# Kernel tuning notes

Measured on AMD Instinct MI355X. Metric: run time of the kernel, lower is better.

The kernel has to match this reference:

```python
import jax, jax.numpy as jnp
import numpy as np

B, S, H, I, E, K = 4, 2048, 1024, 4096, 8, 2


def setup_inputs() -> dict:
    key = jax.random.key(0)
    ks = jax.random.split(key, 5)
    scale = 1.0 / np.sqrt(H)
    return {
        "hidden_states": jax.random.normal(ks[0], (B, S, H), dtype=jnp.float32),
        "router_w": jax.random.normal(ks[1], (E, H), dtype=jnp.float32) * scale,
        "gate_w": jax.random.normal(ks[2], (E, I, H), dtype=jnp.float32) * scale,
        "up_w": jax.random.normal(ks[3], (E, I, H), dtype=jnp.float32) * scale,
        "down_w": jax.random.normal(ks[4], (E, H, I), dtype=jnp.float32) * (1.0 / np.sqrt(I)),
        "top_k": K,
    }


def reference(hidden_states, router_w, gate_w, up_w, down_w, top_k):
    # Router: logits -> softmax -> top-k -> renormalized weights (eval mode, no jitter)
    logits = jnp.einsum("bsh,eh->bse", hidden_states, router_w)
    probs = jax.nn.softmax(logits, axis=-1)
    expert_weights, expert_indices = jax.lax.top_k(probs, top_k)  # [B,S,K]
    expert_weights = expert_weights / expert_weights.sum(axis=-1, keepdims=True)

    n_experts = router_w.shape[0]
    # Per-token combine weight for each expert: [B,S,E]
    combine = (jax.nn.one_hot(expert_indices, n_experts, dtype=expert_weights.dtype)
               * expert_weights[..., None]).sum(axis=-2)

    out = jnp.zeros_like(hidden_states)
    for e in range(n_experts):  # fixed small expert count
        g = jax.nn.silu(hidden_states @ gate_w[e].T)  # [B,S,I]
        u = hidden_states @ up_w[e].T                 # [B,S,I]
        y = (g * u) @ down_w[e].T                     # [B,S,H]
        out = out + combine[..., e:e + 1] * y
    return out
```

## Files before the change

kernel.cpp:

```cpp
#include <hip/hip_runtime.h>
#include <hip/hip_bf16.h>
#include <math.h>
#include <stdint.h>

#define TOKENS 8192
#define HD 1024
#define ID 4096
#define NE 8
#define RMAX 18432
#define MAXT 72

typedef __attribute__((ext_vector_type(8))) short short8v;
typedef __attribute__((ext_vector_type(4))) float f32x4;

typedef const __attribute__((address_space(1))) unsigned int* gas_u32p;
typedef __attribute__((address_space(3))) unsigned int* las_u32p;

__device__ __forceinline__ void stage16(const void* g, void* l) {
  __builtin_amdgcn_global_load_lds((gas_u32p)g, (las_u32p)l, 16, 0, 0);
}

#define BARRIER asm volatile("s_barrier" ::: "memory")
#define WAITLGKM asm volatile("s_waitcnt lgkmcnt(0)" ::: "memory")
#define VMC0 asm volatile("s_waitcnt vmcnt(0)" ::: "memory")
#define VMC3 asm volatile("s_waitcnt vmcnt(3)" ::: "memory")
#define VMC6 asm volatile("s_waitcnt vmcnt(6)" ::: "memory")

__global__ __launch_bounds__(256) void convert_kernel(const float* __restrict__ src,
                                                      __hip_bfloat16* __restrict__ dst) {
  size_t i = ((size_t)blockIdx.x * 256 + threadIdx.x) * 8;
  float4 a = ((const float4*)(src + i))[0];
  float4 b = ((const float4*)(src + i))[1];
  union { __hip_bfloat16 h[8]; int4 v; } u;
  u.h[0] = __float2bfloat16(a.x); u.h[1] = __float2bfloat16(a.y);
  u.h[2] = __float2bfloat16(a.z); u.h[3] = __float2bfloat16(a.w);
  u.h[4] = __float2bfloat16(b.x); u.h[5] = __float2bfloat16(b.y);
  u.h[6] = __float2bfloat16(b.z); u.h[7] = __float2bfloat16(b.w);
  *(int4*)(dst + i) = u.v;
}

__global__ __launch_bounds__(256) void router_kernel(
    const float* __restrict__ h, const float* __restrict__ rw,
    __hip_bfloat16* __restrict__ hx, int* __restrict__ tidx,
    float* __restrict__ tw, int* __restrict__ cnt) {
  int wid = threadIdx.x >> 6, lane = threadIdx.x & 63;
  int t = blockIdx.x * 4 + wid;
  const float4* h4 = (const float4*)(h + (size_t)t * HD);
  float x[16];
  {
    float4 xa = h4[lane * 4 + 0], xb = h4[lane * 4 + 1], xc = h4[lane * 4 + 2], xd = h4[lane * 4 + 3];
    x[0] = xa.x; x[1] = xa.y; x[2] = xa.z; x[3] = xa.w;
    x[4] = xb.x; x[5] = xb.y; x[6] = xb.z; x[7] = xb.w;
    x[8] = xc.x; x[9] = xc.y; x[10] = xc.z; x[11] = xc.w;
    x[12] = xd.x; x[13] = xd.y; x[14] = xd.z; x[15] = xd.w;
  }
  union { __hip_bfloat16 hb[16]; int4 v[2]; } u;
#pragma unroll
  for (int j = 0; j < 16; j++) u.hb[j] = __float2bfloat16(x[j]);
  {
    int4* hxp = (int4*)(hx + (size_t)t * HD + lane * 16);
    hxp[0] = u.v[0]; hxp[1] = u.v[1];
  }
  double acc[NE];
#pragma unroll
  for (int e = 0; e < NE; e++) {
    const float4* w4 = (const float4*)(rw + e * HD);
    float4 wa = w4[lane * 4 + 0], wb = w4[lane * 4 + 1], wc = w4[lane * 4 + 2], wd = w4[lane * 4 + 3];
    double s = 0.0;
    s += (double)x[0] * wa.x + (double)x[1] * wa.y + (double)x[2] * wa.z + (double)x[3] * wa.w;
    s += (double)x[4] * wb.x + (double)x[5] * wb.y + (double)x[6] * wb.z + (double)x[7] * wb.w;
    s += (double)x[8] * wc.x + (double)x[9] * wc.y + (double)x[10] * wc.z + (double)x[11] * wc.w;
    s += (double)x[12] * wd.x + (double)x[13] * wd.y + (double)x[14] * wd.z + (double)x[15] * wd.w;
    acc[e] = s;
  }
#pragma unroll
  for (int off = 32; off >= 1; off >>= 1)
#pragma unroll
    for (int e = 0; e < NE; e++) acc[e] += __shfl_xor(acc[e], off, 64);
  if (lane == 0) {
    int i0 = 0; double l0 = acc[0];
#pragma unroll
    for (int e = 1; e < NE; e++) if (acc[e] > l0) { l0 = acc[e]; i0 = e; }
    int i1 = -1; double l1 = -1.0e300;
#pragma unroll
    for (int e = 0; e < NE; e++) if (e != i0 && acc[e] > l1) { l1 = acc[e]; i1 = e; }
    double r = exp(l1 - l0);
    float w0 = (float)(1.0 / (1.0 + r));
    float w1 = (float)(r / (1.0 + r));
    tidx[t * 2 + 0] = i0; tidx[t * 2 + 1] = i1;
    tw[t * 2 + 0] = w0;  tw[t * 2 + 1] = w1;
    atomicAdd(&cnt[i0], 1); atomicAdd(&cnt[i1], 1);
  }
}

__global__ void scan_kernel(const int* __restrict__ cnt, int* __restrict__ ofs, int* __restrict__ cnt2) {
  if (threadIdx.x == 0) {
    int a = 0;
    for (int e = 0; e < NE; e++) { ofs[e] = a; a += (cnt[e] + 255) & ~255; }
    ofs[NE] = a;
  }
  if (threadIdx.x < NE) cnt2[threadIdx.x] = 0;
}

__global__ __launch_bounds__(256) void scatter_kernel(
    const int* __restrict__ tidx, const float* __restrict__ tw,
    const int* __restrict__ ofs, int* __restrict__ cnt2,
    int* __restrict__ rowmap, int* __restrict__ slots) {
  int t = blockIdx.x * 256 + threadIdx.x;
#pragma unroll
  for (int k = 0; k < 2; k++) {
    int e = tidx[t * 2 + k];
    int pos = atomicAdd(&cnt2[e], 1);
    int row = ofs[e] + pos;
    rowmap[row] = t;
    slots[t * 2 + k] = row;
  }
}

#define MFMAQ(ACC, MO, NO, AF, BF)                                                         \
  { _Pragma("unroll") for (int m_ = 0; m_ < 4; m_++)                                       \
    _Pragma("unroll") for (int n_ = 0; n_ < 2; n_++)                                       \
    _Pragma("unroll") for (int k_ = 0; k_ < 2; k_++)                                       \
      ACC[(MO) + m_][(NO) + n_] = __builtin_amdgcn_mfma_f32_16x16x32_bf16(                 \
          AF[m_][k_], BF[n_][k_], ACC[(MO) + m_][(NO) + n_], 0, 0, 0); }

__global__ __launch_bounds__(512, 2) void gemm1_kernel(
    const __hip_bfloat16* __restrict__ hx, const __hip_bfloat16* __restrict__ Wg,
    const __hip_bfloat16* __restrict__ Wu, const int* __restrict__ rowmap,
    const int* __restrict__ ofs, const __hip_bfloat16* __restrict__ zrow,
    __hip_bfloat16* __restrict__ act) {
  __shared__ __align__(128) char lds[131072];
  const int nwg = gridDim.x;
  int wg0 = blockIdx.x;
  int wg = (wg0 & 7) * (nwg >> 3) + (wg0 >> 3);
  const int tm = wg >> 5, tn = wg & 31;
  const int Rtot = ofs[NE];
  const int row0 = tm * 256;
  if (row0 >= Rtot) return;
  int e = 0;
#pragma unroll
  for (int i = 1; i < NE; i++) e += (row0 >= ofs[i]);
  const int tid = threadIdx.x, wid = tid >> 6, lane = tid & 63;
  const int wm = wid >> 1, wn = wid & 1;
  const int fr = lane & 15, fkE = (lane >> 4) << 3;
  const int wmB = wm * 64, wnB = wn * 64;

  const char* srcA[4]; const char* srcG[2]; const char* srcU[2];
  int ldA[4], ldG[2], ldU[2];
#pragma unroll
  for (int j = 0; j < 4; j++) {
    int d = j * 8192 + tid * 16;
    int row = d >> 7;
    int kb = (d ^ (((d >> 7) & 7) << 4)) & 127;
    int tok = rowmap[row0 + row];
    const __hip_bfloat16* base = (tok >= 0) ? (hx + (size_t)tok * HD) : zrow;
    srcA[j] = (const char*)base + kb;
    ldA[j] = j * 8192 + wid * 1024;
  }
#pragma unroll
  for (int j = 0; j < 2; j++) {
    int d = j * 8192 + tid * 16;
    int row = d >> 7;
    int kb = (d ^ (((d >> 7) & 7) << 4)) & 127;
    srcG[j] = (const char*)(Wg + ((size_t)e * ID + tn * 128 + row) * HD) + kb;
    srcU[j] = (const char*)(Wu + ((size_t)e * ID + tn * 128 + row) * HD) + kb;
    ldG[j] = 32768 + j * 8192 + wid * 1024;
    ldU[j] = 49152 + j * 8192 + wid * 1024;
  }
#define STG_A(j, t, bf) stage16(srcA[j] + (size_t)(t) * 128, (char*)lds + (bf) * 65536 + ldA[j])
#define STG_G(j, t, bf) stage16(srcG[j] + (size_t)(t) * 128, (char*)lds + (bf) * 65536 + ldG[j])
#define STG_U(j, t, bf) stage16(srcU[j] + (size_t)(t) * 128, (char*)lds + (bf) * 65536 + ldU[j])

  auto RD = [&](int bf, int poff, int rowi, int kki) -> short8v {
    int o = ((rowi + fr) << 7) + ((kki << 5) + fkE) * 2;
    o ^= ((o >> 7) & 7) << 4;
    return *(const short8v*)(&lds[bf * 65536 + poff + o]);
  };

  f32x4 accG[4][4], accU[4][4];
#pragma unroll
  for (int m = 0; m < 4; m++)
#pragma unroll
    for (int n = 0; n < 4; n++) { accG[m][n] = (f32x4)(0.0f); accU[m][n] = (f32x4)(0.0f); }

  const int NT = HD / 64;
#pragma unroll
  for (int j = 0; j < 4; j++) STG_A(j, 0, 0);
#pragma unroll
  for (int j = 0; j < 2; j++) STG_G(j, 0, 0);
#pragma unroll
  for (int j = 0; j < 2; j++) STG_U(j, 0, 0);
#pragma unroll
  for (int j = 0; j < 4; j++) STG_A(j, 1, 1);
#pragma unroll
  for (int j = 0; j < 2; j++) STG_G(j, 1, 1);
  VMC6; BARRIER;

#pragma unroll 1
  for (int I = 0; I < NT / 2; ++I) {
    const int t0 = 2 * I;
    const bool more = (t0 + 2 < NT);
    short8v a[4][2], bA[2][2], bB[2][2];
#pragma unroll
    for (int m = 0; m < 4; m++) { a[m][0] = RD(0, 0, wmB + m * 16, 0); a[m][1] = RD(0, 0, wmB + m * 16, 1); }
#pragma unroll
    for (int n = 0; n < 2; n++) { bA[n][0] = RD(0, 32768, wnB + n * 16, 0); bA[n][1] = RD(0, 32768, wnB + n * 16, 1); }
    STG_U(0, t0 + 1, 1); STG_U(1, t0 + 1, 1);
    BARRIER; WAITLGKM;
    __builtin_amdgcn_s_setprio(1); MFMAQ(accG, 0, 0, a, bA); __builtin_amdgcn_s_setprio(0);
    BARRIER;
#pragma unroll
    for (int n = 0; n < 2; n++) { bB[n][0] = RD(0, 32768, wnB + 32 + n * 16, 0); bB[n][1] = RD(0, 32768, wnB + 32 + n * 16, 1); }
    if (more) { STG_A(0, t0 + 2, 0); STG_A(1, t0 + 2, 0); }
    BARRIER; WAITLGKM;
    __builtin_amdgcn_s_setprio(1); MFMAQ(accG, 0, 2, a, bB); __builtin_amdgcn_s_setprio(0);
    BARRIER;
#pragma unroll
    for (int n = 0; n < 2; n++) { bA[n][0] = RD(0, 49152, wnB + n * 16, 0); bA[n][1] = RD(0, 49152, wnB + n * 16, 1); }
    if (more) { STG_A(2, t0 + 2, 0); STG_A(3, t0 + 2, 0); }
    BARRIER; WAITLGKM;
    __builtin_amdgcn_s_setprio(1); MFMAQ(accU, 0, 0, a, bA); __builtin_amdgcn_s_setprio(0);
    BARRIER;
#pragma unroll
    for (int n = 0; n < 2; n++) { bB[n][0] = RD(0, 49152, wnB + 32 + n * 16, 0); bB[n][1] = RD(0, 49152, wnB + 32 + n * 16, 1); }
    if (more) { STG_G(0, t0 + 2, 0); STG_G(1, t0 + 2, 0); }
    BARRIER; WAITLGKM;
    __builtin_amdgcn_s_setprio(1); MFMAQ(accU, 0, 2, a, bB); __builtin_amdgcn_s_setprio(0);
    if (more) { VMC6; } else { VMC0; }
    BARRIER;
#pragma unroll
    for (int m = 0; m < 4; m++) { a[m][0] = RD(1, 0, wmB + m * 16, 0); a[m][1] = RD(1, 0, wmB + m * 16, 1); }
#pragma unroll
    for (int n = 0; n < 2; n++) { bA[n][0] = RD(1, 32768, wnB + n * 16, 0); bA[n][1] = RD(1, 32768, wnB + n * 16, 1); }
    if (more) { STG_U(0, t0 + 2, 0); STG_U(1, t0 + 2, 0); }
    BARRIER; WAITLGKM;
    __builtin_amdgcn_s_setprio(1); MFMAQ(accG, 0, 0, a, bA); __builtin_amdgcn_s_setprio(0);
    BARRIER;
#pragma unroll
    for (int n = 0; n < 2; n++) { bB[n][0] = RD(1, 32768, wnB + 32 + n * 16, 0); bB[n][1] = RD(1, 32768, wnB + 32 + n * 16, 1); }
    if (more) { STG_A(0, t0 + 3, 1); STG_A(1, t0 + 3, 1); }
    BARRIER; WAITLGKM;
    __builtin_amdgcn_s_setprio(1); MFMAQ(accG, 0, 2, a, bB); __builtin_amdgcn_s_setprio(0);
    BARRIER;
#pragma unroll
    for (int n = 0; n < 2; n++) { bA[n][0] = RD(1, 49152, wnB + n * 16, 0); bA[n][1] = RD(1, 49152, wnB + n * 16, 1); }
    if (more) { STG_A(2, t0 + 3, 1); STG_A(3, t0 + 3, 1); }
    BARRIER; WAITLGKM;
    __builtin_amdgcn_s_setprio(1); MFMAQ(accU, 0, 0, a, bA); __builtin_amdgcn_s_setprio(0);
    BARRIER;
#pragma unroll
    for (int n = 0; n < 2; n++) { bB[n][0] = RD(1, 49152, wnB + 32 + n * 16, 0); bB[n][1] = RD(1, 49152, wnB + 32 + n * 16, 1); }
    if (more) { STG_G(0, t0 + 3, 1); STG_G(1, t0 + 3, 1); }
    BARRIER; WAITLGKM;
    __builtin_amdgcn_s_setprio(1); MFMAQ(accU, 0, 2, a, bB); __builtin_amdgcn_s_setprio(0);
    if (more) { VMC6; } else { VMC0; }
    BARRIER;
  }
#undef STG_A
#undef STG_G
#undef STG_U

  const int rb = row0 + wmB + ((lane >> 4) << 2);
  const int cb = tn * 128 + wnB + fr;
#pragma unroll
  for (int m = 0; m < 4; m++)
#pragma unroll
    for (int i = 0; i < 4; i++) {
      int r = rb + m * 16 + i;
      __hip_bfloat16* dst = act + (size_t)r * ID + cb;
#pragma unroll
      for (int n = 0; n < 4; n++) {
        float g = accG[m][n][i], uu = accU[m][n][i];
        float s = g / (1.0f + __expf(-g));
        dst[n * 16] = __float2bfloat16(s * uu);
      }
    }
}

__global__ __launch_bounds__(512, 2) void gemm2_kernel(
    const __hip_bfloat16* __restrict__ act, const __hip_bfloat16* __restrict__ Wd,
    const int* __restrict__ ofs, float* __restrict__ ybuf) {
  __shared__ __align__(128) char lds[98304];
  const int nwg = gridDim.x;
  int wg0 = blockIdx.x;
  int wg = (wg0 & 7) * (nwg >> 3) + (wg0 >> 3);
  const int tm = wg >> 3, tn = wg & 7;
  const int Rtot = ofs[NE];
  const int row0 = tm * 256;
  if (row0 >= Rtot) return;
  int e = 0;
#pragma unroll
  for (int i = 1; i < NE; i++) e += (row0 >= ofs[i]);
  const int tid = threadIdx.x, wid = tid >> 6, lane = tid & 63;
  const int wm = wid >> 1, wn = wid & 1;
  const int fr = lane & 15, fkE = (lane >> 4) << 3;
  const int wmB = wm * 64, wnB = wn * 64;

  const char* srcA[4]; const char* srcB[2];
  int ldA[4], ldB[2];
#pragma unroll
  for (int j = 0; j < 4; j++) {
    int d = j * 8192 + tid * 16;
    int row = d >> 7;
    int kb = (d ^ (((d >> 7) & 7) << 4)) & 127;
    srcA[j] = (const char*)(act + (size_t)(row0 + row) * ID) + kb;
    ldA[j] = j * 8192 + wid * 1024;
  }
#pragma unroll
  for (int j = 0; j < 2; j++) {
    int d = j * 8192 + tid * 16;
    int row = d >> 7;
    int kb = (d ^ (((d >> 7) & 7) << 4)) & 127;
    srcB[j] = (const char*)(Wd + ((size_t)e * HD + tn * 128 + row) * ID) + kb;
    ldB[j] = 32768 + j * 8192 + wid * 1024;
  }
#define STG_A2(j, t, bf) stage16(srcA[j] + (size_t)(t) * 128, (char*)lds + (bf) * 49152 + ldA[j])
#define STG_B2(j, t, bf) stage16(srcB[j] + (size_t)(t) * 128, (char*)lds + (bf) * 49152 + ldB[j])

  auto RD = [&](int bf, int poff, int rowi, int kki) -> short8v {
    int o = ((rowi + fr) << 7) + ((kki << 5) + fkE) * 2;
    o ^= ((o >> 7) & 7) << 4;
    return *(const short8v*)(&lds[bf * 49152 + poff + o]);
  };

  f32x4 acc[4][4];
#pragma unroll
  for (int m = 0; m < 4; m++)
#pragma unroll
    for (int n = 0; n < 4; n++) acc[m][n] = (f32x4)(0.0f);

  const int NT = ID / 64;
#pragma unroll
  for (int j = 0; j < 4; j++) STG_A2(j, 0, 0);
  STG_B2(0, 0, 0); STG_B2(1, 0, 0);
  STG_A2(0, 1, 1); STG_A2(1, 1, 1); STG_A2(2, 1, 1);
  VMC3; BARRIER;

#pragma unroll 1
  for (int I = 0; I < NT / 2; ++I) {
    const int T = 2 * I;
    const bool more = (T + 2 < NT);
    short8v a[4][2], b0[2][2], b1[2][2];
#pragma unroll
    for (int m = 0; m < 4; m++) { a[m][0] = RD(0, 0, wmB + m * 16, 0); a[m][1] = RD(0, 0, wmB + m * 16, 1); }
#pragma unroll
    for (int n = 0; n < 2; n++) { b0[n][0] = RD(0, 32768, wnB + n * 16, 0); b0[n][1] = RD(0, 32768, wnB + n * 16, 1); }
    STG_A2(3, T + 1, 1); STG_B2(0, T + 1, 1); STG_B2(1, T + 1, 1);
    BARRIER; WAITLGKM;
    __builtin_amdgcn_s_setprio(1); MFMAQ(acc, 0, 0, a, b0); __builtin_amdgcn_s_setprio(0);
    BARRIER;
#pragma unroll
    for (int n = 0; n < 2; n++) { b1[n][0] = RD(0, 32768, wnB + 32 + n * 16, 0); b1[n][1] = RD(0, 32768, wnB + 32 + n * 16, 1); }
    if (more) { STG_A2(0, T + 2, 0); STG_A2(1, T + 2, 0); STG_A2(2, T + 2, 0); }
    BARRIER; WAITLGKM;
    __builtin_amdgcn_s_setprio(1); MFMAQ(acc, 0, 2, a, b1); __builtin_amdgcn_s_setprio(0);
    if (more) { VMC3; } else { VMC0; }
    BARRIER;
#pragma unroll
    for (int m = 0; m < 4; m++) { a[m][0] = RD(1, 0, wmB + m * 16, 0); a[m][1] = RD(1, 0, wmB + m * 16, 1); }
#pragma unroll
    for (int n = 0; n < 2; n++) { b0[n][0] = RD(1, 32768, wnB + n * 16, 0); b0[n][1] = RD(1, 32768, wnB + n * 16, 1); }
    if (more) { STG_A2(3, T + 2, 0); STG_B2(0, T + 2, 0); STG_B2(1, T + 2, 0); }
    BARRIER; WAITLGKM;
    __builtin_amdgcn_s_setprio(1); MFMAQ(acc, 0, 0, a, b0); __builtin_amdgcn_s_setprio(0);
    BARRIER;
#pragma unroll
    for (int n = 0; n < 2; n++) { b1[n][0] = RD(1, 32768, wnB + 32 + n * 16, 0); b1[n][1] = RD(1, 32768, wnB + 32 + n * 16, 1); }
    if (more) { STG_A2(0, T + 3, 1); STG_A2(1, T + 3, 1); STG_A2(2, T + 3, 1); }
    BARRIER; WAITLGKM;
    __builtin_amdgcn_s_setprio(1); MFMAQ(acc, 0, 2, a, b1); __builtin_amdgcn_s_setprio(0);
    if (more) { VMC3; } else { VMC0; }
    BARRIER;
  }
#undef STG_A2
#undef STG_B2

  const int rb = row0 + wmB + ((lane >> 4) << 2);
  const int cb = tn * 128 + wnB + fr;
#pragma unroll
  for (int m = 0; m < 4; m++)
#pragma unroll
    for (int i = 0; i < 4; i++) {
      int r = rb + m * 16 + i;
      float* dst = ybuf + (size_t)r * HD + cb;
#pragma unroll
      for (int n = 0; n < 4; n++) dst[n * 16] = acc[m][n][i];
    }
}

__global__ __launch_bounds__(256) void combine_kernel(
    const float* __restrict__ ybuf, const int* __restrict__ slots,
    const float* __restrict__ tw, float* __restrict__ out) {
  int t = blockIdx.x * 4 + (threadIdx.x >> 6);
  int lane = threadIdx.x & 63;
  int r0 = slots[t * 2 + 0], r1 = slots[t * 2 + 1];
  float w0 = tw[t * 2 + 0], w1 = tw[t * 2 + 1];
  const float4* y0 = (const float4*)(ybuf + (size_t)r0 * HD);
  const float4* y1 = (const float4*)(ybuf + (size_t)r1 * HD);
  float4* o = (float4*)(out + (size_t)t * HD);
#pragma unroll
  for (int j = 0; j < 4; j++) {
    int ix = j * 64 + lane;
    float4 a = y0[ix], b = y1[ix];
    float4 c;
    c.x = w0 * a.x + w1 * b.x; c.y = w0 * a.y + w1 * b.y;
    c.z = w0 * a.z + w1 * b.z; c.w = w0 * a.w + w1 * b.w;
    o[ix] = c;
  }
}

extern "C" void kernel_launch(void* const* d_in, const int* in_sizes, int n_in,
                              void* d_out, int out_size, void* d_ws, size_t ws_size,
                              hipStream_t stream) {
  (void)in_sizes; (void)n_in; (void)out_size; (void)ws_size;
  const float* h  = (const float*)d_in[0];
  const float* rw = (const float*)d_in[1];
  const float* gw = (const float*)d_in[2];
  const float* uw = (const float*)d_in[3];
  const float* dw = (const float*)d_in[4];
  float* out = (float*)d_out;

  char* ws = (char*)d_ws;
  size_t off = 0;
  auto alloc = [&](size_t bytes) { char* p = ws + off; off += (bytes + 255) & ~255ULL; return p; };
  __hip_bfloat16* wg  = (__hip_bfloat16*)alloc((size_t)NE * ID * HD * 2);
  __hip_bfloat16* wu  = (__hip_bfloat16*)alloc((size_t)NE * ID * HD * 2);
  __hip_bfloat16* wd  = (__hip_bfloat16*)alloc((size_t)NE * HD * ID * 2);
  __hip_bfloat16* act = (__hip_bfloat16*)alloc((size_t)RMAX * ID * 2);
  __hip_bfloat16* hx  = (__hip_bfloat16*)alloc((size_t)TOKENS * HD * 2);
  float* ybuf = (float*)alloc((size_t)RMAX * HD * 4);
  __hip_bfloat16* zrow = (__hip_bfloat16*)alloc(HD * 2);
  int* rowmap = (int*)alloc(RMAX * 4);
  int* tidx   = (int*)alloc(TOKENS * 2 * 4);
  float* twt  = (float*)alloc(TOKENS * 2 * 4);
  int* slots  = (int*)alloc(TOKENS * 2 * 4);
  int* cnt    = (int*)alloc(256);
  int* cnt2   = (int*)alloc(256);
  int* ofs    = (int*)alloc(256);

  hipMemsetAsync(cnt, 0, NE * 4, stream);
  hipMemsetAsync(rowmap, 0xFF, RMAX * 4, stream);
  hipMemsetAsync(zrow, 0, HD * 2, stream);

  convert_kernel<<<16384, 256, 0, stream>>>(gw, wg);
  convert_kernel<<<16384, 256, 0, stream>>>(uw, wu);
  convert_kernel<<<16384, 256, 0, stream>>>(dw, wd);
  router_kernel<<<TOKENS / 4, 256, 0, stream>>>(h, rw, hx, tidx, twt, cnt);
  scan_kernel<<<1, 64, 0, stream>>>(cnt, ofs, cnt2);
  scatter_kernel<<<TOKENS / 256, 256, 0, stream>>>(tidx, twt, ofs, cnt2, rowmap, slots);
  gemm1_kernel<<<MAXT * 32, 512, 0, stream>>>(hx, wg, wu, rowmap, ofs, zrow, act);
  gemm2_kernel<<<MAXT * 8, 512, 0, stream>>>(act, wd, ofs, ybuf);
  combine_kernel<<<TOKENS / 4, 256, 0, stream>>>(ybuf, slots, twt, out);
}
```

Before: 898.1 us.

## Fuse weight conversions into router and gemm1, triple-buffer gemm2 pipeline

The gate and up weight fp32-to-bf16 conversions move into the router kernel as extra blocks, and the down-weight conversion rides in the gemm1 launch as trailing blocks. This removes three separate launches and lets the conversion overlap with routing and GEMM work. gemm1's tile mapping changes to M-fastest ordering. gemm2 moves from a two-buffer, two-step loop to a three-buffer one-tile-per-iteration pipeline with deeper prefetch, which raises LDS use to 144KB and lowers occupancy.

```diff
diff --git a/kernel.cpp b/kernel.cpp
--- a/kernel.cpp
+++ b/kernel.cpp
@@ -9,6 +9,10 @@
 #define NE 8
 #define RMAX 18432
 #define MAXT 72
+#define NG1 2304
+#define CVTD_BLOCKS 8192
+#define RTR_BLOCKS 2048
+#define CVTGU_BLOCKS 32768
 
 typedef __attribute__((ext_vector_type(8))) short short8v;
 typedef __attribute__((ext_vector_type(4))) float f32x4;
@@ -23,26 +27,30 @@
 #define BARRIER asm volatile("s_barrier" ::: "memory")
 #define WAITLGKM asm volatile("s_waitcnt lgkmcnt(0)" ::: "memory")
 #define VMC0 asm volatile("s_waitcnt vmcnt(0)" ::: "memory")
-#define VMC3 asm volatile("s_waitcnt vmcnt(3)" ::: "memory")
 #define VMC6 asm volatile("s_waitcnt vmcnt(6)" ::: "memory")
 
-__global__ __launch_bounds__(256) void convert_kernel(const float* __restrict__ src,
-                                                      __hip_bfloat16* __restrict__ dst) {
-  size_t i = ((size_t)blockIdx.x * 256 + threadIdx.x) * 8;
-  float4 a = ((const float4*)(src + i))[0];
-  float4 b = ((const float4*)(src + i))[1];
-  union { __hip_bfloat16 h[8]; int4 v; } u;
-  u.h[0] = __float2bfloat16(a.x); u.h[1] = __float2bfloat16(a.y);
-  u.h[2] = __float2bfloat16(a.z); u.h[3] = __float2bfloat16(a.w);
-  u.h[4] = __float2bfloat16(b.x); u.h[5] = __float2bfloat16(b.y);
-  u.h[6] = __float2bfloat16(b.z); u.h[7] = __float2bfloat16(b.w);
-  *(int4*)(dst + i) = u.v;
-}
-
-__global__ __launch_bounds__(256) void router_kernel(
+__global__ __launch_bounds__(256) void router_conv_kernel(
     const float* __restrict__ h, const float* __restrict__ rw,
     __hip_bfloat16* __restrict__ hx, int* __restrict__ tidx,
-    float* __restrict__ tw, int* __restrict__ cnt) {
+    float* __restrict__ tw, int* __restrict__ cnt,
+    const float* __restrict__ gw, const float* __restrict__ uw,
+    __hip_bfloat16* __restrict__ wgu) {
+  if (blockIdx.x >= RTR_BLOCKS) {
+    int cb = blockIdx.x - RTR_BLOCKS;
+    int r = cb >> 14;
+    const float* src = (r == 0) ? gw : uw;
+    __hip_bfloat16* dst = wgu + (size_t)r * ((size_t)NE * ID * HD);
+    size_t i = (((size_t)(cb & 16383)) * 256 + threadIdx.x) * 8;
+    float4 a = ((const float4*)(src + i))[0];
+    float4 b = ((const float4*)(src + i))[1];
+    union { __hip_bfloat16 hh[8]; int4 v; } u;
+    u.hh[0] = __float2bfloat16(a.x); u.hh[1] = __float2bfloat16(a.y);
+    u.hh[2] = __float2bfloat16(a.z); u.hh[3] = __float2bfloat16(a.w);
+    u.hh[4] = __float2bfloat16(b.x); u.hh[5] = __float2bfloat16(b.y);
+    u.hh[6] = __float2bfloat16(b.z); u.hh[7] = __float2bfloat16(b.w);
+    *(int4*)(dst + i) = u.v;
+    return;
+  }
   int wid = threadIdx.x >> 6, lane = threadIdx.x & 63;
   int t = blockIdx.x * 4 + wid;
   const float4* h4 = (const float4*)(h + (size_t)t * HD);
@@ -103,8 +111,7 @@
 }
 
 __global__ __launch_bounds__(256) void scatter_kernel(
-    const int* __restrict__ tidx, const float* __restrict__ tw,
-    const int* __restrict__ ofs, int* __restrict__ cnt2,
+    const int* __restrict__ tidx, const int* __restrict__ ofs, int* __restrict__ cnt2,
     int* __restrict__ rowmap, int* __restrict__ slots) {
   int t = blockIdx.x * 256 + threadIdx.x;
 #pragma unroll
@@ -124,23 +131,42 @@
       ACC[(MO) + m_][(NO) + n_] = __builtin_amdgcn_mfma_f32_16x16x32_bf16(                 \
           AF[m_][k_], BF[n_][k_], ACC[(MO) + m_][(NO) + n_], 0, 0, 0); }
 
+#define MFMA16K(ACC, AF, BF)                                                               \
+  { _Pragma("unroll") for (int m_ = 0; m_ < 4; m_++)                                       \
+    _Pragma("unroll") for (int n_ = 0; n_ < 4; n_++)                                       \
+      ACC[m_][n_] = __builtin_amdgcn_mfma_f32_16x16x32_bf16(                               \
+          AF[m_], BF[n_], ACC[m_][n_], 0, 0, 0); }
+
 __global__ __launch_bounds__(512, 2) void gemm1_kernel(
     const __hip_bfloat16* __restrict__ hx, const __hip_bfloat16* __restrict__ Wg,
     const __hip_bfloat16* __restrict__ Wu, const int* __restrict__ rowmap,
     const int* __restrict__ ofs, const __hip_bfloat16* __restrict__ zrow,
-    __hip_bfloat16* __restrict__ act) {
+    __hip_bfloat16* __restrict__ act,
+    const float* __restrict__ dwsrc, __hip_bfloat16* __restrict__ wd) {
+  const int tid = threadIdx.x;
+  if (blockIdx.x >= NG1) {
+    size_t i = (((size_t)(blockIdx.x - NG1)) * 512 + tid) * 8;
+    float4 a = ((const float4*)(dwsrc + i))[0];
+    float4 b = ((const float4*)(dwsrc + i))[1];
+    union { __hip_bfloat16 h[8]; int4 v; } u;
+    u.h[0] = __float2bfloat16(a.x); u.h[1] = __float2bfloat16(a.y);
+    u.h[2] = __float2bfloat16(a.z); u.h[3] = __float2bfloat16(a.w);
+    u.h[4] = __float2bfloat16(b.x); u.h[5] = __float2bfloat16(b.y);
+    u.h[6] = __float2bfloat16(b.z); u.h[7] = __float2bfloat16(b.w);
+    *(int4*)(wd + i) = u.v;
+    return;
+  }
   __shared__ __align__(128) char lds[131072];
-  const int nwg = gridDim.x;
   int wg0 = blockIdx.x;
-  int wg = (wg0 & 7) * (nwg >> 3) + (wg0 >> 3);
-  const int tm = wg >> 5, tn = wg & 31;
+  int wg = (wg0 & 7) * (NG1 >> 3) + (wg0 >> 3);
+  const int tm = wg % MAXT, tn = wg / MAXT;
   const int Rtot = ofs[NE];
   const int row0 = tm * 256;
   if (row0 >= Rtot) return;
   int e = 0;
 #pragma unroll
   for (int i = 1; i < NE; i++) e += (row0 >= ofs[i]);
-  const int tid = threadIdx.x, wid = tid >> 6, lane = tid & 63;
+  const int wid = tid >> 6, lane = tid & 63;
   const int wm = wid >> 1, wn = wid & 1;
   const int fr = lane & 15, fkE = (lane >> 4) << 3;
   const int wmB = wm * 64, wnB = wn * 64;
@@ -280,7 +306,7 @@
 __global__ __launch_bounds__(512, 2) void gemm2_kernel(
     const __hip_bfloat16* __restrict__ act, const __hip_bfloat16* __restrict__ Wd,
     const int* __restrict__ ofs, float* __restrict__ ybuf) {
-  __shared__ __align__(128) char lds[98304];
+  __shared__ __align__(128) char lds[147456];
   const int nwg = gridDim.x;
   int wg0 = blockIdx.x;
   int wg = (wg0 & 7) * (nwg >> 3) + (wg0 >> 3);
@@ -314,13 +340,13 @@
     srcB[j] = (const char*)(Wd + ((size_t)e * HD + tn * 128 + row) * ID) + kb;
     ldB[j] = 32768 + j * 8192 + wid * 1024;
   }
-#define STG_A2(j, t, bf) stage16(srcA[j] + (size_t)(t) * 128, (char*)lds + (bf) * 49152 + ldA[j])
-#define STG_B2(j, t, bf) stage16(srcB[j] + (size_t)(t) * 128, (char*)lds + (bf) * 49152 + ldB[j])
-
-  auto RD = [&](int bf, int poff, int rowi, int kki) -> short8v {
+#define STG_A2(j, t, q) stage16(srcA[j] + (size_t)(t) * 128, (char*)lds + (q) * 49152 + ldA[j])
+#define STG_B2(j, t, q) stage16(srcB[j] + (size_t)(t) * 128, (char*)lds + (q) * 49152 + ldB[j])
+
+  auto RD = [&](const char* base, int poff, int rowi, int kki) -> short8v {
     int o = ((rowi + fr) << 7) + ((kki << 5) + fkE) * 2;
     o ^= ((o >> 7) & 7) << 4;
-    return *(const short8v*)(&lds[bf * 49152 + poff + o]);
+    return *(const short8v*)(base + poff + o);
   };
 
   f32x4 acc[4][4];
@@ -333,44 +359,36 @@
 #pragma unroll
   for (int j = 0; j < 4; j++) STG_A2(j, 0, 0);
   STG_B2(0, 0, 0); STG_B2(1, 0, 0);
-  STG_A2(0, 1, 1); STG_A2(1, 1, 1); STG_A2(2, 1, 1);
-  VMC3; BARRIER;
-
+#pragma unroll
+  for (int j = 0; j < 4; j++) STG_A2(j, 1, 1);
+  STG_B2(0, 1, 1); STG_B2(1, 1, 1);
+  VMC6; BARRIER;
+
+  int q = 0;
 #pragma unroll 1
-  for (int I = 0; I < NT / 2; ++I) {
-    const int T = 2 * I;
+  for (int T = 0; T < NT; ++T) {
     const bool more = (T + 2 < NT);
-    short8v a[4][2], b0[2][2], b1[2][2];
-#pragma unroll
-    for (int m = 0; m < 4; m++) { a[m][0] = RD(0, 0, wmB + m * 16, 0); a[m][1] = RD(0, 0, wmB + m * 16, 1); }
-#pragma unroll
-    for (int n = 0; n < 2; n++) { b0[n][0] = RD(0, 32768, wnB + n * 16, 0); b0[n][1] = RD(0, 32768, wnB + n * 16, 1); }
-    STG_A2(3, T + 1, 1); STG_B2(0, T + 1, 1); STG_B2(1, T + 1, 1);
-    BARRIER; WAITLGKM;
-    __builtin_amdgcn_s_setprio(1); MFMAQ(acc, 0, 0, a, b0); __builtin_amdgcn_s_setprio(0);
-    BARRIER;
-#pragma unroll
-    for (int n = 0; n < 2; n++) { b1[n][0] = RD(0, 32768, wnB + 32 + n * 16, 0); b1[n][1] = RD(0, 32768, wnB + 32 + n * 16, 1); }
-    if (more) { STG_A2(0, T + 2, 0); STG_A2(1, T + 2, 0); STG_A2(2, T + 2, 0); }
-    BARRIER; WAITLGKM;
-    __builtin_amdgcn_s_setprio(1); MFMAQ(acc, 0, 2, a, b1); __builtin_amdgcn_s_setprio(0);
-    if (more) { VMC3; } else { VMC0; }
-    BARRIER;
-#pragma unroll
-    for (int m = 0; m < 4; m++) { a[m][0] = RD(1, 0, wmB + m * 16, 0); a[m][1] = RD(1, 0, wmB + m * 16, 1); }
-#pragma unroll
-    for (int n = 0; n < 2; n++) { b0[n][0] = RD(1, 32768, wnB + n * 16, 0); b0[n][1] = RD(1, 32768, wnB + n * 16, 1); }
-    if (more) { STG_A2(3, T + 2, 0); STG_B2(0, T + 2, 0); STG_B2(1, T + 2, 0); }
-    BARRIER; WAITLGKM;
-    __builtin_amdgcn_s_setprio(1); MFMAQ(acc, 0, 0, a, b0); __builtin_amdgcn_s_setprio(0);
-    BARRIER;
-#pragma unroll
-    for (int n = 0; n < 2; n++) { b1[n][0] = RD(1, 32768, wnB + 32 + n * 16, 0); b1[n][1] = RD(1, 32768, wnB + 32 + n * 16, 1); }
-    if (more) { STG_A2(0, T + 3, 1); STG_A2(1, T + 3, 1); STG_A2(2, T + 3, 1); }
-    BARRIER; WAITLGKM;
-    __builtin_amdgcn_s_setprio(1); MFMAQ(acc, 0, 2, a, b1); __builtin_amdgcn_s_setprio(0);
-    if (more) { VMC3; } else { VMC0; }
-    BARRIER;
+    const int sq = (q >= 1) ? (q - 1) : 2;
+    const char* base = (const char*)lds + q * 49152;
+    short8v a0[4], b0[4], a1[4], b1[4];
+#pragma unroll
+    for (int m = 0; m < 4; m++) a0[m] = RD(base, 0, wmB + m * 16, 0);
+#pragma unroll
+    for (int n = 0; n < 4; n++) b0[n] = RD(base, 32768, wnB + n * 16, 0);
+    if (more) { STG_A2(0, T + 2, sq); STG_A2(1, T + 2, sq); STG_A2(2, T + 2, sq); }
+    BARRIER; WAITLGKM;
+    __builtin_amdgcn_s_setprio(1); MFMA16K(acc, a0, b0); __builtin_amdgcn_s_setprio(0);
+    BARRIER;
+#pragma unroll
+    for (int m = 0; m < 4; m++) a1[m] = RD(base, 0, wmB + m * 16, 1);
+#pragma unroll
+    for (int n = 0; n < 4; n++) b1[n] = RD(base, 32768, wnB + n * 16, 1);
+    if (more) { STG_A2(3, T + 2, sq); STG_B2(0, T + 2, sq); STG_B2(1, T + 2, sq); }
+    BARRIER; WAITLGKM;
+    __builtin_amdgcn_s_setprio(1); MFMA16K(acc, a1, b1); __builtin_amdgcn_s_setprio(0);
+    if (more) { VMC6; } else { VMC0; }
+    BARRIER;
+    q = (q == 2) ? 0 : (q + 1);
   }
 #undef STG_A2
 #undef STG_B2
@@ -442,13 +460,11 @@
   hipMemsetAsync(rowmap, 0xFF, RMAX * 4, stream);
   hipMemsetAsync(zrow, 0, HD * 2, stream);
 
-  convert_kernel<<<16384, 256, 0, stream>>>(gw, wg);
-  convert_kernel<<<16384, 256, 0, stream>>>(uw, wu);
-  convert_kernel<<<16384, 256, 0, stream>>>(dw, wd);
-  router_kernel<<<TOKENS / 4, 256, 0, stream>>>(h, rw, hx, tidx, twt, cnt);
+  router_conv_kernel<<<RTR_BLOCKS + CVTGU_BLOCKS, 256, 0, stream>>>(
+      h, rw, hx, tidx, twt, cnt, gw, uw, wg);
   scan_kernel<<<1, 64, 0, stream>>>(cnt, ofs, cnt2);
-  scatter_kernel<<<TOKENS / 256, 256, 0, stream>>>(tidx, twt, ofs, cnt2, rowmap, slots);
-  gemm1_kernel<<<MAXT * 32, 512, 0, stream>>>(hx, wg, wu, rowmap, ofs, zrow, act);
+  scatter_kernel<<<TOKENS / 256, 256, 0, stream>>>(tidx, ofs, cnt2, rowmap, slots);
+  gemm1_kernel<<<NG1 + CVTD_BLOCKS, 512, 0, stream>>>(hx, wg, wu, rowmap, ofs, zrow, act, dw, wd);
   gemm2_kernel<<<MAXT * 8, 512, 0, stream>>>(act, wd, ofs, ybuf);
   combine_kernel<<<TOKENS / 4, 256, 0, stream>>>(ybuf, slots, twt, out);
 }
```

Measured after the change: 833.8 us. 7.2% less time.
